# Kernel optimization log

Hardware: AMD Instinct MI355X
Metric: run time of the kernel (lower is better)

The kernel has to match this reference:

```python
import jax, jax.numpy as jnp
import numpy as np

NEG_INF = -1000000000.0

def setup_inputs() -> dict:
    key = jax.random.key(0)
    k1, k2, k3, k4 = jax.random.split(key, 4)
    B, H, S, D = 4, 16, 2048, 64
    Q = jax.random.normal(k1, (B, H, S, D), dtype=jnp.float32)
    K = jax.random.normal(k2, (B, H, S, D), dtype=jnp.float32)
    V = jax.random.normal(k3, (B, H, S, D), dtype=jnp.float32)
    mask = jax.random.randint(k4, (B, H, S, S), 0, 2, dtype=jnp.int32)
    return {"Q": Q, "K": K, "V": V, "mask": mask, "scale": 8}

def reference(Q, K, V, mask, scale):
    # scores: [B,H,S,S]
    scores = jnp.einsum('bhqd,bhkd->bhqk', Q, K)
    scores = scores / scale
    scores = jnp.where(mask == 0, NEG_INF, scores)
    attention = jax.nn.softmax(scores, axis=-1)
    output = jnp.einsum('bhqk,bhkd->bhqd', attention, V)
    return (output, attention)
```

## Files before the change

### kernel.cpp

```cpp
#include <hip/hip_runtime.h>
#include <hip/hip_bf16.h>

#define S_LEN 2048
#define D_DIM 64
#define TQ    16
#define SROW  2056

typedef __bf16 bf16x8 __attribute__((ext_vector_type(8)));
typedef __bf16 bf16x4 __attribute__((ext_vector_type(4)));
typedef float  f32x4  __attribute__((ext_vector_type(4)));

__global__ __launch_bounds__(256, 2)
void sdpa_kernel(const float* __restrict__ Q, const float* __restrict__ K,
                 const float* __restrict__ V, const int* __restrict__ mask,
                 const int* __restrict__ scale_p,
                 float* __restrict__ out, float* __restrict__ att)
{
    __shared__ __bf16 Ss[TQ][SROW];

    const int tid  = threadIdx.x;
    const int lane = tid & 63;
    const int wv   = tid >> 6;
    const int lm   = lane & 15;
    const int lq   = lane >> 4;

    const int qt = blockIdx.x;
    const int bh = blockIdx.y;
    const int q0 = qt * TQ;

    const float rscale = 1.0f / (float)(*scale_p);

    bf16x8 qf[2];
    {
        const float* qp = Q + ((size_t)bh * S_LEN + q0 + lm) * D_DIM + lq * 8;
        #pragma unroll
        for (int c = 0; c < 2; ++c) {
            float4 a = *(const float4*)(qp + c * 32);
            float4 b = *(const float4*)(qp + c * 32 + 4);
            qf[c][0] = (__bf16)(a.x * rscale); qf[c][1] = (__bf16)(a.y * rscale);
            qf[c][2] = (__bf16)(a.z * rscale); qf[c][3] = (__bf16)(a.w * rscale);
            qf[c][4] = (__bf16)(b.x * rscale); qf[c][5] = (__bf16)(b.y * rscale);
            qf[c][6] = (__bf16)(b.z * rscale); qf[c][7] = (__bf16)(b.w * rscale);
        }
    }

    {
        const float* kb = K + (size_t)bh * S_LEN * D_DIM;
        const int key0 = wv * (S_LEN / 4);
        for (int t = 0; t < 32; ++t) {
            const int kt = key0 + t * 16;
            const float* kp = kb + (size_t)(kt + lm) * D_DIM + lq * 8;
            f32x4 acc = {0.f, 0.f, 0.f, 0.f};
            #pragma unroll
            for (int c = 0; c < 2; ++c) {
                float4 a = *(const float4*)(kp + c * 32);
                float4 b = *(const float4*)(kp + c * 32 + 4);
                bf16x8 kf;
                kf[0] = (__bf16)a.x; kf[1] = (__bf16)a.y;
                kf[2] = (__bf16)a.z; kf[3] = (__bf16)a.w;
                kf[4] = (__bf16)b.x; kf[5] = (__bf16)b.y;
                kf[6] = (__bf16)b.z; kf[7] = (__bf16)b.w;
                acc = __builtin_amdgcn_mfma_f32_16x16x32_bf16(qf[c], kf, acc, 0, 0, 0);
            }
            const int col = kt + lm;
            #pragma unroll
            for (int i = 0; i < 4; ++i)
                Ss[lq * 4 + i][col] = (__bf16)acc[i];
        }
    }
    __syncthreads();

    const int r = tid >> 4;
    const int g = tid & 15;

    float rmax;
    {
        const int* mp = mask + ((size_t)bh * S_LEN + q0 + r) * S_LEN;
        float mx = -3.0e38f;
        for (int k = 0; k < 32; ++k) {
            const int c = g * 4 + k * 64;
            int4 mv = *(const int4*)(mp + c);
            bf16x4 sv = *(const bf16x4*)(&Ss[r][c]);
            bf16x4 so;
            so[0] = (mv.x == 0) ? (__bf16)(-1.0e9f) : sv[0];
            so[1] = (mv.y == 0) ? (__bf16)(-1.0e9f) : sv[1];
            so[2] = (mv.z == 0) ? (__bf16)(-1.0e9f) : sv[2];
            so[3] = (mv.w == 0) ? (__bf16)(-1.0e9f) : sv[3];
            *(bf16x4*)(&Ss[r][c]) = so;
            mx = fmaxf(mx, fmaxf(fmaxf((float)so[0], (float)so[1]),
                                 fmaxf((float)so[2], (float)so[3])));
        }
        #pragma unroll
        for (int off = 8; off > 0; off >>= 1)
            mx = fmaxf(mx, __shfl_xor(mx, off));
        rmax = mx;
    }

    float rl;
    {
        float sum = 0.f;
        for (int k = 0; k < 32; ++k) {
            const int c = g * 4 + k * 64;
            bf16x4 sv = *(const bf16x4*)(&Ss[r][c]);
            sum += __expf((float)sv[0] - rmax);
            sum += __expf((float)sv[1] - rmax);
            sum += __expf((float)sv[2] - rmax);
            sum += __expf((float)sv[3] - rmax);
        }
        #pragma unroll
        for (int off = 8; off > 0; off >>= 1)
            sum += __shfl_xor(sum, off);
        rl = 1.0f / sum;
    }

    {
        float* ap = att + ((size_t)bh * S_LEN + q0 + r) * S_LEN;
        for (int k = 0; k < 32; ++k) {
            const int c = g * 4 + k * 64;
            bf16x4 sv = *(const bf16x4*)(&Ss[r][c]);
            float4 p;
            p.x = __expf((float)sv[0] - rmax) * rl;
            p.y = __expf((float)sv[1] - rmax) * rl;
            p.z = __expf((float)sv[2] - rmax) * rl;
            p.w = __expf((float)sv[3] - rmax) * rl;
            *(float4*)(ap + c) = p;
            bf16x4 pb;
            pb[0] = (__bf16)p.x; pb[1] = (__bf16)p.y;
            pb[2] = (__bf16)p.z; pb[3] = (__bf16)p.w;
            *(bf16x4*)(&Ss[r][c]) = pb;
        }
    }
    __syncthreads();

    {
        const float* vb = V + (size_t)bh * S_LEN * D_DIM + wv * 16 + lm;
        f32x4 o = {0.f, 0.f, 0.f, 0.f};
        for (int kc = 0; kc < 64; ++kc) {
            bf16x8 af = *(const bf16x8*)(&Ss[lm][kc * 32 + lq * 8]);
            const float* vp = vb + (size_t)(kc * 32 + lq * 8) * D_DIM;
            bf16x8 bfr;
            #pragma unroll
            for (int j = 0; j < 8; ++j)
                bfr[j] = (__bf16)vp[(size_t)j * D_DIM];
            o = __builtin_amdgcn_mfma_f32_16x16x32_bf16(af, bfr, o, 0, 0, 0);
        }
        float* op = out + ((size_t)bh * S_LEN + q0 + lq * 4) * D_DIM + wv * 16 + lm;
        #pragma unroll
        for (int i = 0; i < 4; ++i)
            op[(size_t)i * D_DIM] = o[i];
    }
}

extern "C" void kernel_launch(void* const* d_in, const int* in_sizes, int n_in,
                              void* d_out, int out_size, void* d_ws, size_t ws_size,
                              hipStream_t stream) {
    const float* Q    = (const float*)d_in[0];
    const float* K    = (const float*)d_in[1];
    const float* V    = (const float*)d_in[2];
    const int*   mask = (const int*)d_in[3];
    const int*   sc   = (const int*)d_in[4];
    float* out = (float*)d_out;
    float* att = out + (size_t)4 * 16 * S_LEN * D_DIM;

    dim3 grid(S_LEN / TQ, 4 * 16);
    sdpa_kernel<<<grid, 256, 0, stream>>>(Q, K, V, mask, sc, out, att);
}
```

Before: 2.392 ms.

## Fuse masking and online softmax statistics into the QK^T MFMA loop

Applies the mask and computes running row max and sum (online softmax) directly in the score-producing loop. The statistics are merged across lanes with shuffles and across waves through small shared arrays. This removes the two separate LDS passes over the score tile that computed max and sum. In exchange, the mask is now read as per-lane scalar int loads in a strided pattern instead of int4 vectors, and each score costs an extra exp.

```diff
diff --git a/kernel.cpp b/kernel.cpp
--- a/kernel.cpp
+++ b/kernel.cpp
@@ -17,6 +17,8 @@
                  float* __restrict__ out, float* __restrict__ att)
 {
     __shared__ __bf16 Ss[TQ][SROW];
+    __shared__ float  Mw[4][TQ];
+    __shared__ float  Lw[4][TQ];
 
     const int tid  = threadIdx.x;
     const int lane = tid & 63;
@@ -44,9 +46,14 @@
         }
     }
 
+    float mrow[4], lrow[4];
+    #pragma unroll
+    for (int i = 0; i < 4; ++i) { mrow[i] = -3.0e38f; lrow[i] = 0.f; }
+
     {
         const float* kb = K + (size_t)bh * S_LEN * D_DIM;
         const int key0 = wv * (S_LEN / 4);
+        const int* mp = mask + ((size_t)bh * S_LEN + q0 + lq * 4) * S_LEN + lm;
         for (int t = 0; t < 32; ++t) {
             const int kt = key0 + t * 16;
             const float* kp = kb + (size_t)(kt + lm) * D_DIM + lq * 8;
@@ -64,8 +71,35 @@
             }
             const int col = kt + lm;
             #pragma unroll
-            for (int i = 0; i < 4; ++i)
-                Ss[lq * 4 + i][col] = (__bf16)acc[i];
+            for (int i = 0; i < 4; ++i) {
+                const int mv = mp[(size_t)i * S_LEN + kt];
+                const __bf16 sb = (mv == 0) ? (__bf16)(-1.0e9f) : (__bf16)acc[i];
+                Ss[lq * 4 + i][col] = sb;
+                const float sf = (float)sb;
+                const float d = sf - mrow[i];
+                const float e = __expf(-fabsf(d));
+                lrow[i] = (d <= 0.f) ? (lrow[i] + e) : fmaf(lrow[i], e, 1.0f);
+                mrow[i] = fmaxf(mrow[i], sf);
+            }
+        }
+        #pragma unroll
+        for (int off = 1; off < 16; off <<= 1) {
+            #pragma unroll
+            for (int i = 0; i < 4; ++i) {
+                const float mo = __shfl_xor(mrow[i], off);
+                const float lo = __shfl_xor(lrow[i], off);
+                const float d  = mo - mrow[i];
+                const float e  = __expf(-fabsf(d));
+                lrow[i] = (d <= 0.f) ? fmaf(lo, e, lrow[i]) : fmaf(lrow[i], e, lo);
+                mrow[i] = fmaxf(mrow[i], mo);
+            }
+        }
+        if (lm == 0) {
+            #pragma unroll
+            for (int i = 0; i < 4; ++i) {
+                Mw[wv][lq * 4 + i] = mrow[i];
+                Lw[wv][lq * 4 + i] = lrow[i];
+            }
         }
     }
     __syncthreads();
@@ -73,44 +107,19 @@
     const int r = tid >> 4;
     const int g = tid & 15;
 
-    float rmax;
+    float rmax, rl;
     {
-        const int* mp = mask + ((size_t)bh * S_LEN + q0 + r) * S_LEN;
-        float mx = -3.0e38f;
-        for (int k = 0; k < 32; ++k) {
-            const int c = g * 4 + k * 64;
-            int4 mv = *(const int4*)(mp + c);
-            bf16x4 sv = *(const bf16x4*)(&Ss[r][c]);
-            bf16x4 so;
-            so[0] = (mv.x == 0) ? (__bf16)(-1.0e9f) : sv[0];
-            so[1] = (mv.y == 0) ? (__bf16)(-1.0e9f) : sv[1];
-            so[2] = (mv.z == 0) ? (__bf16)(-1.0e9f) : sv[2];
-            so[3] = (mv.w == 0) ? (__bf16)(-1.0e9f) : sv[3];
-            *(bf16x4*)(&Ss[r][c]) = so;
-            mx = fmaxf(mx, fmaxf(fmaxf((float)so[0], (float)so[1]),
-                                 fmaxf((float)so[2], (float)so[3])));
+        float M = Mw[0][r], L = Lw[0][r];
+        #pragma unroll
+        for (int w = 1; w < 4; ++w) {
+            const float mo = Mw[w][r], lo = Lw[w][r];
+            const float d  = mo - M;
+            const float e  = __expf(-fabsf(d));
+            L = (d <= 0.f) ? fmaf(lo, e, L) : fmaf(L, e, lo);
+            M = fmaxf(M, mo);
         }
-        #pragma unroll
-        for (int off = 8; off > 0; off >>= 1)
-            mx = fmaxf(mx, __shfl_xor(mx, off));
-        rmax = mx;
-    }
-
-    float rl;
-    {
-        float sum = 0.f;
-        for (int k = 0; k < 32; ++k) {
-            const int c = g * 4 + k * 64;
-            bf16x4 sv = *(const bf16x4*)(&Ss[r][c]);
-            sum += __expf((float)sv[0] - rmax);
-            sum += __expf((float)sv[1] - rmax);
-            sum += __expf((float)sv[2] - rmax);
-            sum += __expf((float)sv[3] - rmax);
-        }
-        #pragma unroll
-        for (int off = 8; off > 0; off >>= 1)
-            sum += __shfl_xor(sum, off);
-        rl = 1.0f / sum;
+        rmax = M;
+        rl = 1.0f / L;
     }
 
     {
```

After: 2.378 ms. Within noise of the previous version (-0.6%).
